# Performance work log

Measured on AMD Instinct MI355X. Metric: run time of the kernel, lower is better.

Reference implementation:

```python
import jax, jax.numpy as jnp
import numpy as np

INDEX_SHIFT = jnp.array([[0, 0], [-1, 0], [1, 0], [0, 1], [-1, 1], [1, 1], [0, -1], [-1, -1], [1, -1]], dtype=jnp.int32)
GRID = jnp.array([513, 513], dtype=jnp.int32)  # pseudo_image_dims + 1


def setup_inputs() -> dict:
    key = jax.random.key(0)
    k1, k2, k3, k4 = jax.random.split(key, 4)
    li_bev_coors = jax.random.randint(k1, (8192, 2), 0, 512, dtype=jnp.int32)
    ra_bev_coors = jax.random.randint(k2, (2048, 2), 0, 512, dtype=jnp.int32)
    ra_pts = jax.random.normal(k3, (2048, 5), dtype=jnp.float32)
    ra_voxel_coords = jax.random.randint(k4, (2048, 3), 0, 512, dtype=jnp.int32)
    return {"li_bev_coors": li_bev_coors, "ra_bev_coors": ra_bev_coors,
            "ra_pts": ra_pts, "ra_voxel_coords": ra_voxel_coords}


def _neighbour_coors(bev_grids):
    # [N,2] -> [N,9,2]: shift by 9-neighborhood, wrap by (grid_size+1)
    return (bev_grids[:, None, :] + INDEX_SHIFT[None, :, :]) % GRID


def _nearest_dy(neighbour_coor, dy_coor, dy_mask):
    # neighbour_coor: [N,9,2] int; dy_coor: [M,2] float; dy_mask: [M] bool
    n = neighbour_coor.shape[0]
    a = neighbour_coor.reshape(-1, 2).astype(jnp.float32)        # [N*9, 2]
    a2 = jnp.sum(a * a, axis=-1)                                  # [N*9]
    b2 = jnp.sum(dy_coor * dy_coor, axis=-1)                      # [M]
    # squared euclidean distances (exact: integer coordinates)
    d2 = a2[:, None] + b2[None, :] - 2.0 * (a @ dy_coor.T)        # [N*9, M]
    d2 = jnp.where(dy_mask[None, :], d2, jnp.inf)                 # mask non-dynamic voxels
    dmin = jnp.sqrt(jnp.maximum(jnp.min(d2, axis=-1), 0.0))       # min commutes with sqrt
    return (dmin * 0.01).reshape(n, 9)


def reference(li_bev_coors, ra_bev_coors, ra_pts, ra_voxel_coords):
    # dynamic-point selection: |velocity| > 0.1 (column 4)
    dy_mask = jnp.abs(ra_pts[:, 4]) > 0.1                         # [M]
    dy_coor = ra_voxel_coords[:, 1:].astype(jnp.float32)          # [M,2]
    # (uniquifying dy_coor does not change the min-distance; skip for jit shapes)
    li_nb = _neighbour_coors(li_bev_coors)                        # [N_li,9,2]
    ra_nb = _neighbour_coors(ra_bev_coors)                        # [N_ra,9,2]
    use = jnp.sum(dy_mask) > 1
    li_dis = jnp.where(use, _nearest_dy(li_nb, dy_coor, dy_mask), 0.0)
    ra_dis = jnp.where(use, _nearest_dy(ra_nb, dy_coor, dy_mask), 0.0)
    return (li_dis, ra_dis)
```

## Files before the change

kernel.cpp:

```cpp
#include <hip/hip_runtime.h>

#define BLOCK 256
#define SPLITS 8
#define MAXC 264

__device__ __forceinline__ float d2f(float qx, float qy, float cx, float cy) {
    float dx = qx - cx;
    float dy = qy - cy;
    return fmaf(dx, dx, dy * dy);
}

__global__ __launch_bounds__(BLOCK) void partial_kernel(
    const int* __restrict__ li_coors, int n_li,
    const int* __restrict__ ra_coors, int n_ra,
    const float* __restrict__ pts,
    const int* __restrict__ vox,
    int m, int cs, int csPad,
    int* __restrict__ out_bits,
    int* __restrict__ counter)
{
    __shared__ float2 sc[MAXC];

    const int base = blockIdx.y * cs;
    int nvalid = 0;
    for (int i = threadIdx.x; i < csPad; i += BLOCK) {
        int gi = base + i;
        float x = 3.0e4f, y = 3.0e4f;
        bool valid = false;
        if (i < cs && gi < m) {
            valid = fabsf(pts[gi * 5 + 4]) > 0.1f;
            if (valid) { x = (float)vox[gi * 3 + 1]; y = (float)vox[gi * 3 + 2]; }
        }
        sc[i] = make_float2(x, y);
        nvalid += valid ? 1 : 0;
    }
    if (blockIdx.x == 0 && nvalid) atomicAdd(counter, nvalid);
    __syncthreads();

    const int li_total = n_li * 9;
    const int total = (n_li + n_ra) * 9;
    const int q = blockIdx.x * BLOCK + threadIdx.x;
    if (q >= total) return;

    const int shift_x[9] = {0,-1,1,0,-1,1,0,-1,1};
    const int shift_y[9] = {0, 0,0,1, 1,1,-1,-1,-1};
    int n, s;
    const int* __restrict__ src;
    if (q < li_total) { n = q / 9; s = q - n * 9; src = li_coors; }
    else { int r = q - li_total; n = r / 9; s = r - n * 9; src = ra_coors; }

    int cx = src[n * 2 + 0] + shift_x[s];
    int cy = src[n * 2 + 1] + shift_y[s];
    if (cx < 0) cx += 513;
    if (cy < 0) cy += 513;
    const float qx = (float)cx;
    const float qy = (float)cy;

    const float4* __restrict__ s4 = (const float4*)sc;
    float m0 = 3.4e38f, m1 = 3.4e38f, m2 = 3.4e38f, m3 = 3.4e38f;
    const int iters = csPad >> 3;
    for (int i = 0; i < iters; ++i) {
        float4 a = s4[4 * i + 0];
        float4 b = s4[4 * i + 1];
        float4 c = s4[4 * i + 2];
        float4 d = s4[4 * i + 3];
        m0 = fminf(m0, d2f(qx, qy, a.x, a.y));
        m1 = fminf(m1, d2f(qx, qy, b.x, b.y));
        m2 = fminf(m2, d2f(qx, qy, c.x, c.y));
        m3 = fminf(m3, d2f(qx, qy, d.x, d.y));
        m0 = fminf(m0, d2f(qx, qy, a.z, a.w));
        m1 = fminf(m1, d2f(qx, qy, b.z, b.w));
        m2 = fminf(m2, d2f(qx, qy, c.z, c.w));
        m3 = fminf(m3, d2f(qx, qy, d.z, d.w));
    }
    float best = fminf(fminf(m0, m1), fminf(m2, m3));

    atomicMin(out_bits + q, __float_as_int(best));
}

__global__ __launch_bounds__(BLOCK) void finalize_kernel(
    float* __restrict__ out, int total, const int* __restrict__ counter)
{
    int q = blockIdx.x * BLOCK + threadIdx.x;
    if (q >= total) return;
    float d2 = out[q];
    int cnt = *counter;
    out[q] = (cnt > 1) ? sqrtf(d2) * 0.01f : 0.0f;
}

extern "C" void kernel_launch(void* const* d_in, const int* in_sizes, int n_in,
                              void* d_out, int out_size, void* d_ws, size_t ws_size,
                              hipStream_t stream) {
    const int*   li  = (const int*)d_in[0];
    const int*   ra  = (const int*)d_in[1];
    const float* pts = (const float*)d_in[2];
    const int*   vox = (const int*)d_in[3];
    float* out = (float*)d_out;
    int*   counter = (int*)d_ws;

    const int n_li = in_sizes[0] / 2;
    const int n_ra = in_sizes[1] / 2;
    const int m    = in_sizes[2] / 5;

    const int total = (n_li + n_ra) * 9;
    const int qblocks = (total + BLOCK - 1) / BLOCK;

    const int cs    = (m + SPLITS - 1) / SPLITS;
    const int csPad = (cs + 7) & ~7;

    hipMemsetAsync(d_out, 0x7F, (size_t)total * sizeof(float), stream);
    hipMemsetAsync(d_ws, 0, sizeof(int), stream);

    dim3 grid(qblocks, SPLITS);
    partial_kernel<<<grid, BLOCK, 0, stream>>>(li, n_li, ra, n_ra, pts, vox,
                                               m, cs, csPad,
                                               (int*)d_out, counter);
    finalize_kernel<<<qblocks, BLOCK, 0, stream>>>(out, total, counter);
}
```

Before: 80.25 us.

## Register-tile queries per thread, expand distance algebraically, reduce splits via partial buffer

Each thread now handles 8 query points, so every shared-memory candidate load serves 8 queries. The squared distance is expanded as c2 - 2q·c with q2 added after the min, which saves arithmetic per pair. Per-split minima are written to a workspace buffer that the finalize kernel reduces, replacing global atomicMin and the output memset. Splits double to 16 to keep the grid large, at the cost of more partial-buffer traffic and a reassociated sum that could differ slightly in floating point.

```diff
diff --git a/kernel.cpp b/kernel.cpp
--- a/kernel.cpp
+++ b/kernel.cpp
@@ -1,14 +1,10 @@
 #include <hip/hip_runtime.h>
 
 #define BLOCK 256
-#define SPLITS 8
+#define SPLITS 16
+#define QPT 8
 #define MAXC 264
 
-__device__ __forceinline__ float d2f(float qx, float qy, float cx, float cy) {
-    float dx = qx - cx;
-    float dy = qy - cy;
-    return fmaf(dx, dx, dy * dy);
-}
 
 __global__ __launch_bounds__(BLOCK) void partial_kernel(
     const int* __restrict__ li_coors, int n_li,
@@ -16,76 +12,91 @@
     const float* __restrict__ pts,
     const int* __restrict__ vox,
     int m, int cs, int csPad,
-    int* __restrict__ out_bits,
+    float* __restrict__ partials,
     int* __restrict__ counter)
 {
     __shared__ float2 sc[MAXC];
 
-    const int base = blockIdx.y * cs;
+    const int split = blockIdx.y;
+    const int base = split * cs;
     int nvalid = 0;
     for (int i = threadIdx.x; i < csPad; i += BLOCK) {
         int gi = base + i;
         float x = 3.0e4f, y = 3.0e4f;
-        bool valid = false;
         if (i < cs && gi < m) {
-            valid = fabsf(pts[gi * 5 + 4]) > 0.1f;
-            if (valid) { x = (float)vox[gi * 3 + 1]; y = (float)vox[gi * 3 + 2]; }
+            if (fabsf(pts[gi * 5 + 4]) > 0.1f) {
+                x = (float)vox[gi * 3 + 1];
+                y = (float)vox[gi * 3 + 2];
+                nvalid++;
+            }
         }
         sc[i] = make_float2(x, y);
-        nvalid += valid ? 1 : 0;
     }
     if (blockIdx.x == 0 && nvalid) atomicAdd(counter, nvalid);
     __syncthreads();
 
     const int li_total = n_li * 9;
     const int total = (n_li + n_ra) * 9;
-    const int q = blockIdx.x * BLOCK + threadIdx.x;
-    if (q >= total) return;
+    const int qbase = blockIdx.x * (BLOCK * QPT) + threadIdx.x;
 
-    const int shift_x[9] = {0,-1,1,0,-1,1,0,-1,1};
-    const int shift_y[9] = {0, 0,0,1, 1,1,-1,-1,-1};
-    int n, s;
-    const int* __restrict__ src;
-    if (q < li_total) { n = q / 9; s = q - n * 9; src = li_coors; }
-    else { int r = q - li_total; n = r / 9; s = r - n * 9; src = ra_coors; }
-
-    int cx = src[n * 2 + 0] + shift_x[s];
-    int cy = src[n * 2 + 1] + shift_y[s];
-    if (cx < 0) cx += 513;
-    if (cy < 0) cy += 513;
-    const float qx = (float)cx;
-    const float qy = (float)cy;
+    float n2x[QPT], n2y[QPT], q2[QPT], m0[QPT], m1[QPT];
+#pragma unroll
+    for (int k = 0; k < QPT; ++k) {
+        int q = qbase + k * BLOCK;
+        float qx = 0.0f, qy = 0.0f;
+        if (q < total) {
+            const int shift_x[9] = {0,-1,1,0,-1,1,0,-1,1};
+            const int shift_y[9] = {0, 0,0,1, 1,1,-1,-1,-1};
+            int n, s;
+            const int* src;
+            if (q < li_total) { n = q / 9; s = q - n * 9; src = li_coors; }
+            else { int r = q - li_total; n = r / 9; s = r - n * 9; src = ra_coors; }
+            int cx = src[n * 2 + 0] + shift_x[s];
+            int cy = src[n * 2 + 1] + shift_y[s];
+            if (cx < 0) cx += 513;
+            if (cy < 0) cy += 513;
+            qx = (float)cx; qy = (float)cy;
+        }
+        n2x[k] = -2.0f * qx;
+        n2y[k] = -2.0f * qy;
+        q2[k]  = fmaf(qx, qx, qy * qy);
+        m0[k] = 3.4e38f; m1[k] = 3.4e38f;
+    }
 
     const float4* __restrict__ s4 = (const float4*)sc;
-    float m0 = 3.4e38f, m1 = 3.4e38f, m2 = 3.4e38f, m3 = 3.4e38f;
-    const int iters = csPad >> 3;
+    const int iters = csPad >> 1;
     for (int i = 0; i < iters; ++i) {
-        float4 a = s4[4 * i + 0];
-        float4 b = s4[4 * i + 1];
-        float4 c = s4[4 * i + 2];
-        float4 d = s4[4 * i + 3];
-        m0 = fminf(m0, d2f(qx, qy, a.x, a.y));
-        m1 = fminf(m1, d2f(qx, qy, b.x, b.y));
-        m2 = fminf(m2, d2f(qx, qy, c.x, c.y));
-        m3 = fminf(m3, d2f(qx, qy, d.x, d.y));
-        m0 = fminf(m0, d2f(qx, qy, a.z, a.w));
-        m1 = fminf(m1, d2f(qx, qy, b.z, b.w));
-        m2 = fminf(m2, d2f(qx, qy, c.z, c.w));
-        m3 = fminf(m3, d2f(qx, qy, d.z, d.w));
+        float4 a = s4[i];
+        float c2a = fmaf(a.x, a.x, a.y * a.y);
+        float c2b = fmaf(a.z, a.z, a.w * a.w);
+#pragma unroll
+        for (int k = 0; k < QPT; ++k) {
+            float ta = fmaf(a.x, n2x[k], fmaf(a.y, n2y[k], c2a));
+            float tb = fmaf(a.z, n2x[k], fmaf(a.w, n2y[k], c2b));
+            m0[k] = fminf(m0[k], ta);
+            m1[k] = fminf(m1[k], tb);
+        }
     }
-    float best = fminf(fminf(m0, m1), fminf(m2, m3));
 
-    atomicMin(out_bits + q, __float_as_int(best));
+    float* __restrict__ dst = partials + (size_t)split * total;
+#pragma unroll
+    for (int k = 0; k < QPT; ++k) {
+        int q = qbase + k * BLOCK;
+        if (q < total) dst[q] = q2[k] + fminf(m0[k], m1[k]);
+    }
 }
 
 __global__ __launch_bounds__(BLOCK) void finalize_kernel(
-    float* __restrict__ out, int total, const int* __restrict__ counter)
+    const float* __restrict__ partials, int total,
+    const int* __restrict__ counter, float* __restrict__ out)
 {
     int q = blockIdx.x * BLOCK + threadIdx.x;
     if (q >= total) return;
-    float d2 = out[q];
-    int cnt = *counter;
-    out[q] = (cnt > 1) ? sqrtf(d2) * 0.01f : 0.0f;
+    float best = 3.4e38f;
+#pragma unroll
+    for (int s = 0; s < SPLITS; ++s)
+        best = fminf(best, partials[(size_t)s * total + q]);
+    out[q] = (*counter > 1) ? sqrtf(best) * 0.01f : 0.0f;
 }
 
 extern "C" void kernel_launch(void* const* d_in, const int* in_sizes, int n_in,
@@ -96,24 +107,25 @@
     const float* pts = (const float*)d_in[2];
     const int*   vox = (const int*)d_in[3];
     float* out = (float*)d_out;
-    int*   counter = (int*)d_ws;
+
+    int*   counter  = (int*)d_ws;
+    float* partials = (float*)((char*)d_ws + 256);
 
     const int n_li = in_sizes[0] / 2;
     const int n_ra = in_sizes[1] / 2;
     const int m    = in_sizes[2] / 5;
 
     const int total = (n_li + n_ra) * 9;
-    const int qblocks = (total + BLOCK - 1) / BLOCK;
+    const int qblocks = (total + BLOCK * QPT - 1) / (BLOCK * QPT);
+    const int fblocks = (total + BLOCK - 1) / BLOCK;
 
     const int cs    = (m + SPLITS - 1) / SPLITS;
     const int csPad = (cs + 7) & ~7;
 
-    hipMemsetAsync(d_out, 0x7F, (size_t)total * sizeof(float), stream);
     hipMemsetAsync(d_ws, 0, sizeof(int), stream);
 
     dim3 grid(qblocks, SPLITS);
     partial_kernel<<<grid, BLOCK, 0, stream>>>(li, n_li, ra, n_ra, pts, vox,
-                                               m, cs, csPad,
-                                               (int*)d_out, counter);
-    finalize_kernel<<<qblocks, BLOCK, 0, stream>>>(out, total, counter);
+                                               m, cs, csPad, partials, counter);
+    finalize_kernel<<<fblocks, BLOCK, 0, stream>>>(partials, total, counter, out);
 }
```

New measurement: 85.87 us. 7.0% more time.
